# Performance work log

Measured on AMD Instinct MI355X. Metric: run time of the kernel, lower is better.

Reference implementation:

```python
import jax, jax.numpy as jnp
import numpy as np

B, T, ENC_H, DEC_H, ATTN = 128, 2048, 512, 512, 128


def setup_inputs() -> dict:
    key = jax.random.key(0)
    k1, k2, k3, k4, k5 = jax.random.split(key, 5)
    s = lambda fan_in: 1.0 / np.sqrt(fan_in)
    return {
        "encoder_outputs": jax.random.normal(k1, (B, T, ENC_H), dtype=jnp.float32),
        "decoder_hidden": jax.random.normal(k2, (B, DEC_H), dtype=jnp.float32),
        # nn.Linear weights are [out_features, in_features]
        "W_enc": jax.random.uniform(k3, (ATTN, ENC_H), jnp.float32, -s(ENC_H), s(ENC_H)),
        "W_dec": jax.random.uniform(k4, (ATTN, DEC_H), jnp.float32, -s(DEC_H), s(DEC_H)),
        "v_w": jax.random.uniform(k5, (1, ATTN), jnp.float32, -s(ATTN), s(ATTN)),
    }


def reference(encoder_outputs, decoder_hidden, W_enc, W_dec, v_w):
    # enc_proj: [B, T, A]
    enc_proj = jnp.einsum("bth,ah->bta", encoder_outputs, W_enc)
    # dec_proj: [B, 1, A]
    dec_proj = jnp.einsum("bh,ah->ba", decoder_hidden, W_dec)[:, None, :]
    energy = jnp.tanh(enc_proj + dec_proj)                      # [B, T, A]
    scores = jnp.einsum("bta,a->bt", energy, v_w[0])            # [B, T]
    weights = jax.nn.softmax(scores, axis=-1)                   # [B, T]
    context = jnp.einsum("bt,bth->bh", weights, encoder_outputs)  # [B, ENC_H]
    return context, weights
```

## Files before the change

### kernel.cpp

```cpp
#include <hip/hip_runtime.h>
#include <hip/hip_bf16.h>

#define B_SZ   128
#define T_SZ   2048
#define ENCH   512
#define ATTN_  128
#define NBLK   256
#define STRIPS_PER_BLK 8

typedef __attribute__((ext_vector_type(8))) short short8;
typedef __attribute__((ext_vector_type(4))) float f32x4;

__device__ __forceinline__ unsigned short f2bf_rne(float f) {
  unsigned u = __builtin_bit_cast(unsigned, f);
  u += 0x7FFFu + ((u >> 16) & 1u);
  return (unsigned short)(u >> 16);
}
__device__ __forceinline__ float fast_tanh(float x) {
  float e = __expf(2.f * x);
  return 1.f - __fdividef(2.f, e + 1.f);
}
__device__ __forceinline__ short8 pack8(float4 a, float4 b) {
  union { unsigned u[4]; short8 s; } r;
  asm("v_cvt_pk_bf16_f32 %0, %1, %2" : "=v"(r.u[0]) : "v"(a.x), "v"(a.y));
  asm("v_cvt_pk_bf16_f32 %0, %1, %2" : "=v"(r.u[1]) : "v"(a.z), "v"(a.w));
  asm("v_cvt_pk_bf16_f32 %0, %1, %2" : "=v"(r.u[2]) : "v"(b.x), "v"(b.y));
  asm("v_cvt_pk_bf16_f32 %0, %1, %2" : "=v"(r.u[3]) : "v"(b.z), "v"(b.w));
  return r.s;
}
template<int CTRL>
__device__ __forceinline__ float dpp_add(float v) {
  int t = __builtin_amdgcn_update_dpp(0, __builtin_bit_cast(int, v),
                                      CTRL, 0xf, 0xf, true);
  return v + __builtin_bit_cast(float, t);
}
__device__ __forceinline__ float sum16(float v) {
  v = dpp_add<0xB1>(v);
  v = dpp_add<0x4E>(v);
  v = dpp_add<0x141>(v);
  v = dpp_add<0x140>(v);
  return v;
}

__global__ void k_convert_wfrag(const float* __restrict__ w,
                                unsigned short* __restrict__ o) {
  int idx = blockIdx.x * 256 + threadIdx.x;
  int l   = idx & 63;
  int wks = idx >> 6;
  int cg  = wks >> 4, ks = wks & 15;
  int row = cg * 16 + (l & 15);
  int col = ks * 32 + (l >> 4) * 8;
  const float4* src = reinterpret_cast<const float4*>(w + row * ENCH + col);
  float4 v0 = src[0], v1 = src[1];
  short8 r;
  r[0] = (short)f2bf_rne(v0.x); r[1] = (short)f2bf_rne(v0.y);
  r[2] = (short)f2bf_rne(v0.z); r[3] = (short)f2bf_rne(v0.w);
  r[4] = (short)f2bf_rne(v1.x); r[5] = (short)f2bf_rne(v1.y);
  r[6] = (short)f2bf_rne(v1.z); r[7] = (short)f2bf_rne(v1.w);
  *reinterpret_cast<short8*>(o + (size_t)idx * 8) = r;
}

__global__ void k_decproj(const float* __restrict__ dec,
                          const float* __restrict__ wdec,
                          float* __restrict__ out) {
  __shared__ float dh[ENCH];
  int b = blockIdx.x, tid = threadIdx.x;
  for (int i = tid; i < ENCH; i += 128) dh[i] = dec[b * ENCH + i];
  __syncthreads();
  const float4* wr4 = reinterpret_cast<const float4*>(wdec + tid * ENCH);
  float acc = 0.f;
  for (int h4 = 0; h4 < ENCH / 4; ++h4) {
    float4 w4 = wr4[h4];
    acc += dh[h4 * 4 + 0] * w4.x + dh[h4 * 4 + 1] * w4.y +
           dh[h4 * 4 + 2] * w4.z + dh[h4 * 4 + 3] * w4.w;
  }
  out[b * ATTN_ + tid] = acc;
}

__global__ __launch_bounds__(512, 2) void k_main(
    const float* __restrict__ enc,
    const unsigned short* __restrict__ wfrag,
    const float* __restrict__ decproj,
    const float* __restrict__ vw,
    float* __restrict__ scores_raw,
    float* __restrict__ ctx_part,
    float* __restrict__ ml_part)
{
  const int tid  = threadIdx.x;
  const int lane = tid & 63;
  const int wid  = tid >> 6;
  const int l15  = lane & 15;
  const int g    = lane >> 4;

  __shared__ unsigned short w_lds[ATTN_ * ENCH];

#pragma unroll
  for (int r = 0; r < 16; ++r) {
    int i = r * 512 + tid;
    reinterpret_cast<short8*>(w_lds)[i] = reinterpret_cast<const short8*>(wfrag)[i];
  }
  float vv[8];
#pragma unroll
  for (int cg = 0; cg < 8; ++cg) vv[cg] = vw[cg * 16 + l15];
  __syncthreads();

#pragma unroll 1
  for (int i = 0; i < STRIPS_PER_BLK; ++i) {
    const int cid = blockIdx.x * STRIPS_PER_BLK + i;
    const int b   = cid >> 4;
    const int s16 = cid & 15;
    const int row0 = s16 * 128 + wid * 16;
    const float* arow = enc + ((size_t)b * T_SZ + row0 + l15) * ENCH + g * 8;

    float4 r0[16], r1[16];
#pragma unroll
    for (int ks = 0; ks < 16; ++ks) {
      r0[ks] = *reinterpret_cast<const float4*>(arow + ks * 32);
      r1[ks] = *reinterpret_cast<const float4*>(arow + ks * 32 + 4);
    }

    float dv[8];
#pragma unroll
    for (int cg = 0; cg < 8; ++cg) dv[cg] = decproj[b * ATTN_ + cg * 16 + l15];

    f32x4 acc[8];
#pragma unroll
    for (int cg = 0; cg < 8; ++cg) acc[cg] = (f32x4){0.f, 0.f, 0.f, 0.f};
#pragma unroll
    for (int ks = 0; ks < 16; ++ks) {
      short8 af = pack8(r0[ks], r1[ks]);
      const char* wb = (const char*)w_lds + ks * 1024 + lane * 16;
#pragma unroll
      for (int cg = 0; cg < 8; ++cg) {
        short8 bf = *reinterpret_cast<const short8*>(wb + cg * 16384);
        acc[cg] = __builtin_amdgcn_mfma_f32_16x16x32_bf16(af, bf, acc[cg], 0, 0, 0);
      }
    }

    float er[4];
#pragma unroll
    for (int r = 0; r < 4; ++r) {
      float e = 0.f;
#pragma unroll
      for (int cg = 0; cg < 8; ++cg)
        e += fast_tanh(acc[cg][r] + dv[cg]) * vv[cg];
      er[r] = sum16(e);
    }
    if (l15 == 0) {
#pragma unroll
      for (int r = 0; r < 4; ++r)
        scores_raw[(size_t)b * T_SZ + row0 + g * 4 + r] = er[r];
    }

    float mg = fmaxf(fmaxf(er[0], er[1]), fmaxf(er[2], er[3]));
    mg = fmaxf(mg, __shfl_xor(mg, 16));
    mg = fmaxf(mg, __shfl_xor(mg, 32));
    float x0 = __expf(er[0] - mg), x1 = __expf(er[1] - mg);
    float x2 = __expf(er[2] - mg), x3 = __expf(er[3] - mg);
    float xs = (x0 + x1) + (x2 + x3);
    xs += __shfl_xor(xs, 16);
    xs += __shfl_xor(xs, 32);
    const float l_run = xs;
    float sel = (l15 & 3) == 0 ? er[0]
              : (l15 & 3) == 1 ? er[1]
              : (l15 & 3) == 2 ? er[2] : er[3];
    float smine = __shfl(sel, ((l15 >> 2) << 4) | (l15 & 3));
    const float p_me = __expf(smine - mg);

    float ctx8[8];
#pragma unroll
    for (int j = 0; j < 8; ++j) ctx8[j] = 0.f;
#pragma unroll
    for (int ks = 0; ks < 16; ++ks) {
      float c[8];
      c[0] = p_me * r0[ks].x; c[1] = p_me * r0[ks].y;
      c[2] = p_me * r0[ks].z; c[3] = p_me * r0[ks].w;
      c[4] = p_me * r1[ks].x; c[5] = p_me * r1[ks].y;
      c[6] = p_me * r1[ks].z; c[7] = p_me * r1[ks].w;
#pragma unroll
      for (int j = 0; j < 8; ++j) c[j] = sum16(c[j]);
      if (l15 == ks) {
#pragma unroll
        for (int j = 0; j < 8; ++j) ctx8[j] = c[j];
      }
    }

    const size_t widx = (size_t)b * 128 + s16 * 8 + wid;
    float* cp = ctx_part + widx * ENCH + l15 * 32 + g * 8;
    *reinterpret_cast<float4*>(cp)     = (float4){ctx8[0], ctx8[1], ctx8[2], ctx8[3]};
    *reinterpret_cast<float4*>(cp + 4) = (float4){ctx8[4], ctx8[5], ctx8[6], ctx8[7]};
    if (lane == 0) {
      ml_part[widx * 2 + 0] = mg;
      ml_part[widx * 2 + 1] = l_run;
    }
  }
}

__global__ void k_combine(const float* __restrict__ ctx_part,
                          const float* __restrict__ ml_part,
                          float* __restrict__ out_ctx,
                          float* __restrict__ weights)
{
  __shared__ float msh[128], lsh[128], fac[128];
  int b = blockIdx.x, tid = threadIdx.x;
  if (tid < 128) {
    msh[tid] = ml_part[((size_t)b * 128 + tid) * 2 + 0];
    lsh[tid] = ml_part[((size_t)b * 128 + tid) * 2 + 1];
  }
  __syncthreads();
  float M = msh[0];
  for (int w = 1; w < 128; ++w) M = fmaxf(M, msh[w]);
  if (tid < 128) fac[tid] = __expf(msh[tid] - M);
  __syncthreads();
  float L = 0.f;
  for (int w = 0; w < 128; ++w) L += fac[w] * lsh[w];
  float Linv = 1.f / L;
  for (int h = tid; h < ENCH; h += 256) {
    float a = 0.f;
    for (int w = 0; w < 128; ++w)
      a += fac[w] * ctx_part[((size_t)b * 128 + w) * ENCH + h];
    out_ctx[b * ENCH + h] = a * Linv;
  }
  for (int t = tid; t < T_SZ; t += 256) {
    float raw = weights[(size_t)b * T_SZ + t];
    weights[(size_t)b * T_SZ + t] = __expf(raw - M) * Linv;
  }
}

extern "C" void kernel_launch(void* const* d_in, const int* in_sizes, int n_in,
                              void* d_out, int out_size, void* d_ws, size_t ws_size,
                              hipStream_t stream) {
  const float* enc  = (const float*)d_in[0];
  const float* dec  = (const float*)d_in[1];
  const float* wenc = (const float*)d_in[2];
  const float* wdec = (const float*)d_in[3];
  const float* vw   = (const float*)d_in[4];

  float* out     = (float*)d_out;
  float* out_ctx = out;
  float* out_w   = out + B_SZ * ENCH;

  char* ws = (char*)d_ws;
  unsigned short* wfrag = (unsigned short*)ws;
  float* decproj  = (float*)(ws + 131072);
  float* ml_part  = (float*)(ws + 131072 + 65536);
  float* ctx_part = (float*)(ws + 131072 + 65536 + 131072);

  hipLaunchKernelGGL(k_convert_wfrag, dim3(32), dim3(256), 0, stream, wenc, wfrag);
  hipLaunchKernelGGL(k_decproj, dim3(B_SZ), dim3(128), 0, stream, dec, wdec, decproj);
  hipLaunchKernelGGL(k_main, dim3(NBLK), dim3(512), 0, stream,
                     enc, wfrag, decproj, vw, out_w, ctx_part, ml_part);
  hipLaunchKernelGGL(k_combine, dim3(B_SZ), dim3(256), 0, stream,
                     ctx_part, ml_part, out_ctx, out_w);
}
```

Measured before the change: 179.4 us.

## Prefetch next strip of encoder rows into registers during context reduction

Each block now handles one batch half (8 consecutive strips), so the decoder projection is loaded once per block and the first strip's encoder rows before the loop. While the context accumulation for the current strip consumes the registers, the loads for the next strip are issued into the same registers, overlapping global memory latency with the DPP reductions and MFMA work. This relies on the compiler keeping the reload ordered after each register's last use, and register pressure stays roughly the same.

```diff
diff --git a/kernel.cpp b/kernel.cpp
--- a/kernel.cpp
+++ b/kernel.cpp
@@ -99,29 +99,33 @@
     int i = r * 512 + tid;
     reinterpret_cast<short8*>(w_lds)[i] = reinterpret_cast<const short8*>(wfrag)[i];
   }
-  float vv[8];
-#pragma unroll
-  for (int cg = 0; cg < 8; ++cg) vv[cg] = vw[cg * 16 + l15];
-  __syncthreads();
+
+  const int b       = blockIdx.x >> 1;
+  const int s16base = (blockIdx.x & 1) * 8;
+  float vv[8], dv[8];
+#pragma unroll
+  for (int cg = 0; cg < 8; ++cg) {
+    vv[cg] = vw[cg * 16 + l15];
+    dv[cg] = decproj[b * ATTN_ + cg * 16 + l15];
+  }
+  __syncthreads();
+
+  const size_t encbase = ((size_t)b * T_SZ + wid * 16 + l15) * ENCH + g * 8;
+
+  float4 r0[16], r1[16];
+  {
+    const float* a0 = enc + encbase + (size_t)(s16base * 128) * ENCH;
+#pragma unroll
+    for (int ks = 0; ks < 16; ++ks) {
+      r0[ks] = *reinterpret_cast<const float4*>(a0 + ks * 32);
+      r1[ks] = *reinterpret_cast<const float4*>(a0 + ks * 32 + 4);
+    }
+  }
 
 #pragma unroll 1
   for (int i = 0; i < STRIPS_PER_BLK; ++i) {
-    const int cid = blockIdx.x * STRIPS_PER_BLK + i;
-    const int b   = cid >> 4;
-    const int s16 = cid & 15;
+    const int s16  = s16base + i;
     const int row0 = s16 * 128 + wid * 16;
-    const float* arow = enc + ((size_t)b * T_SZ + row0 + l15) * ENCH + g * 8;
-
-    float4 r0[16], r1[16];
-#pragma unroll
-    for (int ks = 0; ks < 16; ++ks) {
-      r0[ks] = *reinterpret_cast<const float4*>(arow + ks * 32);
-      r1[ks] = *reinterpret_cast<const float4*>(arow + ks * 32 + 4);
-    }
-
-    float dv[8];
-#pragma unroll
-    for (int cg = 0; cg < 8; ++cg) dv[cg] = decproj[b * ATTN_ + cg * 16 + l15];
 
     f32x4 acc[8];
 #pragma unroll
@@ -170,18 +174,38 @@
     float ctx8[8];
 #pragma unroll
     for (int j = 0; j < 8; ++j) ctx8[j] = 0.f;
-#pragma unroll
-    for (int ks = 0; ks < 16; ++ks) {
-      float c[8];
-      c[0] = p_me * r0[ks].x; c[1] = p_me * r0[ks].y;
-      c[2] = p_me * r0[ks].z; c[3] = p_me * r0[ks].w;
-      c[4] = p_me * r1[ks].x; c[5] = p_me * r1[ks].y;
-      c[6] = p_me * r1[ks].z; c[7] = p_me * r1[ks].w;
-#pragma unroll
-      for (int j = 0; j < 8; ++j) c[j] = sum16(c[j]);
-      if (l15 == ks) {
-#pragma unroll
-        for (int j = 0; j < 8; ++j) ctx8[j] = c[j];
+    if (i + 1 < STRIPS_PER_BLK) {
+      const float* an = enc + encbase + (size_t)((s16 + 1) * 128) * ENCH;
+#pragma unroll
+      for (int ks = 0; ks < 16; ++ks) {
+        float c[8];
+        c[0] = p_me * r0[ks].x; c[1] = p_me * r0[ks].y;
+        c[2] = p_me * r0[ks].z; c[3] = p_me * r0[ks].w;
+        c[4] = p_me * r1[ks].x; c[5] = p_me * r1[ks].y;
+        c[6] = p_me * r1[ks].z; c[7] = p_me * r1[ks].w;
+        r0[ks] = *reinterpret_cast<const float4*>(an + ks * 32);
+        r1[ks] = *reinterpret_cast<const float4*>(an + ks * 32 + 4);
+#pragma unroll
+        for (int j = 0; j < 8; ++j) c[j] = sum16(c[j]);
+        if (l15 == ks) {
+#pragma unroll
+          for (int j = 0; j < 8; ++j) ctx8[j] = c[j];
+        }
+      }
+    } else {
+#pragma unroll
+      for (int ks = 0; ks < 16; ++ks) {
+        float c[8];
+        c[0] = p_me * r0[ks].x; c[1] = p_me * r0[ks].y;
+        c[2] = p_me * r0[ks].z; c[3] = p_me * r0[ks].w;
+        c[4] = p_me * r1[ks].x; c[5] = p_me * r1[ks].y;
+        c[6] = p_me * r1[ks].z; c[7] = p_me * r1[ks].w;
+#pragma unroll
+        for (int j = 0; j < 8; ++j) c[j] = sum16(c[j]);
+        if (l15 == ks) {
+#pragma unroll
+          for (int j = 0; j < 8; ++j) ctx8[j] = c[j];
+        }
       }
     }
 
```

Measured after the change: 239.3 us. +33.4%, slower.
